# Kernel tuning notes

Measured on AMD Instinct MI355X. Metric: run time of the kernel, lower is better.

## Reference

```python
import jax, jax.numpy as jnp
import numpy as np

TEMPERATURE = 0.1
EPS = 1e-8

# MatchingRuleAllViews defaults:
#   intra_view_same_class=1, intra_view_different_class=0,
#   inter_view_same_class=1, inter_view_different_class=0,
#   inter_image_same_class=-1, inter_image_different_class=-1,
#   self_similarity=-1

def setup_inputs() -> dict:
    key = jax.random.key(0)
    k1, k2, k3 = jax.random.split(key, 3)
    B, V, C, HW = 2, 2, 64, 1024
    student = jax.random.normal(k1, (B, V, C, HW), dtype=jnp.float32)
    teacher = jax.random.normal(k2, (B, V, C, HW), dtype=jnp.float32)
    labels = jax.random.randint(k3, (B, V, HW), 0, 5, dtype=jnp.int32)
    return {"student_embeddings": student, "teacher_embeddings": teacher, "labels": labels}


def _masks(B, V, HW, labels_flat):
    # image / view / pixel ids for each of the N = B*V*HW flattened positions
    image_ids = jnp.repeat(jnp.arange(B), V * HW)          # [N]
    view_ids = jnp.tile(jnp.repeat(jnp.arange(V), HW), B)  # [N]
    pixel_ids = jnp.tile(jnp.arange(HW), B * V)            # [N]
    si = image_ids[:, None] == image_ids[None, :]
    sv = view_ids[:, None] == view_ids[None, :]
    sp = pixel_ids[:, None] == pixel_ids[None, :]
    sc = labels_flat[:, None] == labels_flat[None, :]
    # default rule: same image -> (same class ? 1 : 0); different image -> -1;
    # self-similarity (same image, view, pixel) -> -1
    mask = jnp.where(si, jnp.where(sc, 1, 0), -1)
    mask = jnp.where(si & sv & sp, -1, mask)
    numerator_mask = (mask == 1).astype(jnp.float32)
    denom_mask = (mask >= 0).astype(jnp.float32)
    return numerator_mask, denom_mask


def reference(student_embeddings, teacher_embeddings, labels):
    B, V, C, HW = student_embeddings.shape
    N = B * V * HW
    # [B,V,C,HW] -> [N,C], L2-normalized
    sf = student_embeddings.transpose(0, 1, 3, 2).reshape(N, C)
    tf = teacher_embeddings.transpose(0, 1, 3, 2).reshape(N, C)
    sf = sf / jnp.linalg.norm(sf, axis=1, keepdims=True).clip(1e-12)
    tf = tf / jnp.linalg.norm(tf, axis=1, keepdims=True).clip(1e-12)
    logits = (sf @ tf.T) / TEMPERATURE  # [N,N]

    labels_flat = labels.reshape(-1)
    numerator_mask, denom_mask = _masks(B, V, HW, labels_flat)

    # masked log-softmax over dim 1 (denominator restricted to denom_mask)
    masked_logits = jnp.where(denom_mask > 0, logits, -jnp.inf)
    log_prob = jax.nn.log_softmax(masked_logits, axis=1)
    log_prob = jnp.where(jnp.isneginf(log_prob), 0.0, log_prob)

    numerator_sums = numerator_mask.sum(1)
    mean_log_prob_pos = (numerator_mask * log_prob).sum(1) / (numerator_sums + EPS)
    valid = numerator_sums > EPS  # [N] bool
    n_valid = valid.sum().astype(jnp.float32)
    loss = -jnp.sum(jnp.where(valid, mean_log_prob_pos, 0.0)) / n_valid

    # bg_anchors=False branch: (loss * non_bg[valid]).sum() / (non_bg[valid].sum() + eps)
    non_bg = (labels_flat != 0).astype(jnp.float32)
    non_bg_valid_sum = jnp.sum(non_bg * valid.astype(jnp.float32))
    loss = (loss * non_bg_valid_sum) / (non_bg_valid_sum + EPS)
    return loss
```

## Files before the change

kernel.cpp:

```cpp
#include <hip/hip_runtime.h>
#include <math.h>

#define C_DIM 64
#define HW_DIM 1024
#define N_TOT 4096
#define IMG 2048
#define NEG_INF (-1e30f)

__global__ __launch_bounds__(256) void norms_kernel(
    const float* __restrict__ s, const float* __restrict__ t,
    float* __restrict__ rs, float* __restrict__ rt,
    float* __restrict__ accums) {
    const int b = blockIdx.x;
    const int pos = threadIdx.x & 63;
    const int chunk = threadIdx.x >> 6;
    const int n = ((b & 63) << 6) + pos;
    const float* __restrict__ src = (b >= 64) ? t : s;
    const int base = ((n >> 10) << 16) + (n & 1023);
    float ss = 0.f;
#pragma unroll
    for (int k = 0; k < 16; ++k) {
        float a = src[base + ((chunk << 4) + k) * HW_DIM];
        ss = fmaf(a, a, ss);
    }
    __shared__ float red[4][64];
    red[chunk][pos] = ss;
    __syncthreads();
    if (threadIdx.x < 64) {
        float v = red[0][pos] + red[1][pos] + red[2][pos] + red[3][pos];
        float r = 1.f / fmaxf(sqrtf(v), 1e-12f);
        if (b >= 64) rt[n] = r; else rs[n] = r;
    }
    if (b == 0 && threadIdx.x < 8) accums[threadIdx.x] = 0.f;
}

__global__ __launch_bounds__(256, 2) void logits_stats_kernel(
    const float* __restrict__ s, const float* __restrict__ t,
    const int* __restrict__ labels, const float* __restrict__ rs,
    const float* __restrict__ rt, float4* __restrict__ stats) {

    const int rb = blockIdx.x >> 3;
    const int jc = blockIdx.x & 7;
    const int img = rb >> 4;
    const int i0 = rb * 128;
    const int jbase0 = img * IMG + jc * 256;

    const int tid = threadIdx.x;
    const int tx = tid & 15;
    const int ty = tid >> 4;

    __shared__ __align__(16) float lds_a[C_DIM][132];
    __shared__ __align__(16) float lds_b[C_DIM][144];
    __shared__ __align__(16) float lds_rsa[128];
    __shared__ __align__(16) float lds_rtb[256];
    __shared__ __align__(16) int lds_labj[256];

    if (tid < 128) lds_rsa[tid] = rs[i0 + tid];
    lds_rtb[tid] = rt[jbase0 + tid];
    lds_labj[tid] = labels[jbase0 + tid];
    __syncthreads();

    {
        const int bvi = ((i0 >> 10) << 16) + (i0 & 1023);
        const int pos4 = (tid & 31) << 2;
        const int c0 = tid >> 5;
        float4 rv = *(const float4*)&lds_rsa[pos4];
#pragma unroll
        for (int k = 0; k < 8; ++k) {
            int c = c0 + (k << 3);
            float4 v = *(const float4*)(s + bvi + c * HW_DIM + pos4);
            v.x *= rv.x; v.y *= rv.y; v.z *= rv.z; v.w *= rv.w;
            *(float4*)&lds_a[c][pos4] = v;
        }
    }

    int lab_i[8];
#pragma unroll
    for (int rr = 0; rr < 8; ++rr) lab_i[rr] = labels[i0 + ty * 8 + rr];

    float m_run[8], s_run[8], A_run[8], c_run[8];
#pragma unroll
    for (int rr = 0; rr < 8; ++rr) {
        m_run[rr] = NEG_INF; s_run[rr] = 0.f; A_run[rr] = 0.f; c_run[rr] = 0.f;
    }

    const int arow = ty << 3;
    const int bo = tx << 3;
    const int bos = bo + ((bo >> 5) << 2);

    for (int jh = 0; jh < 2; ++jh) {
        const int colh = jh * 128;
        const int jb_img = jbase0 + colh;
        __syncthreads();
        {
            const int bvj = ((jb_img >> 10) << 16) + (jb_img & 1023);
            const int pos4 = (tid & 31) << 2;
            const int c0 = tid >> 5;
            float4 rv = *(const float4*)&lds_rtb[colh + pos4];
            const int sp = pos4 + ((pos4 >> 5) << 2);
#pragma unroll
            for (int k = 0; k < 8; ++k) {
                int c = c0 + (k << 3);
                float4 v = *(const float4*)(t + bvj + c * HW_DIM + pos4);
                v.x *= rv.x; v.y *= rv.y; v.z *= rv.z; v.w *= rv.w;
                *(float4*)&lds_b[c][sp] = v;
            }
        }
        __syncthreads();

        int labj[8];
        {
            int4 l0 = *(const int4*)&lds_labj[colh + bo];
            int4 l1 = *(const int4*)&lds_labj[colh + bo + 4];
            labj[0] = l0.x; labj[1] = l0.y; labj[2] = l0.z; labj[3] = l0.w;
            labj[4] = l1.x; labj[5] = l1.y; labj[6] = l1.z; labj[7] = l1.w;
        }

        float acc[8][8];
#pragma unroll
        for (int a = 0; a < 8; ++a)
#pragma unroll
            for (int b2 = 0; b2 < 8; ++b2) acc[a][b2] = 0.f;

#pragma unroll 4
        for (int c = 0; c < C_DIM; ++c) {
            float4 a0 = *(const float4*)&lds_a[c][arow];
            float4 a1 = *(const float4*)&lds_a[c][arow + 4];
            float4 b0 = *(const float4*)&lds_b[c][bos];
            float4 b1 = *(const float4*)&lds_b[c][bos + 4];
            const float ar[8] = {a0.x, a0.y, a0.z, a0.w, a1.x, a1.y, a1.z, a1.w};
            const float br[8] = {b0.x, b0.y, b0.z, b0.w, b1.x, b1.y, b1.z, b1.w};
#pragma unroll
            for (int a = 0; a < 8; ++a)
#pragma unroll
                for (int b2 = 0; b2 < 8; ++b2)
                    acc[a][b2] = fmaf(ar[a], br[b2], acc[a][b2]);
        }

#pragma unroll
        for (int rr = 0; rr < 8; ++rr) {
            const int i_g = i0 + arow + rr;
            const int li = lab_i[rr];
            float vals[8];
            float lm = NEG_INF;
#pragma unroll
            for (int jj = 0; jj < 8; ++jj) {
                const int j_g = jb_img + bo + jj;
                float logit = acc[rr][jj] * 10.f;
                bool self = (j_g == i_g);
                float v = self ? NEG_INF : logit;
                vals[jj] = v;
                lm = fmaxf(lm, v);
                if (!self && labj[jj] == li) {
                    A_run[rr] += logit;
                    c_run[rr] += 1.f;
                }
            }
            float M = fmaxf(m_run[rr], lm);
            float sn = s_run[rr] * __expf(m_run[rr] - M);
#pragma unroll
            for (int jj = 0; jj < 8; ++jj) sn += __expf(vals[jj] - M);
            m_run[rr] = M;
            s_run[rr] = sn;
        }
    }

#pragma unroll
    for (int off = 1; off < 16; off <<= 1) {
#pragma unroll
        for (int rr = 0; rr < 8; ++rr) {
            float m2 = __shfl_xor(m_run[rr], off, 64);
            float s2 = __shfl_xor(s_run[rr], off, 64);
            float A2 = __shfl_xor(A_run[rr], off, 64);
            float c2 = __shfl_xor(c_run[rr], off, 64);
            float M = fmaxf(m_run[rr], m2);
            s_run[rr] = s_run[rr] * __expf(m_run[rr] - M) + s2 * __expf(m2 - M);
            m_run[rr] = M;
            A_run[rr] += A2;
            c_run[rr] += c2;
        }
    }

    if (tx == 0) {
#pragma unroll
        for (int rr = 0; rr < 8; ++rr) {
            const int i_g = i0 + arow + rr;
            stats[i_g * 8 + jc] = make_float4(m_run[rr], s_run[rr], A_run[rr], c_run[rr]);
        }
    }
}

__global__ __launch_bounds__(256) void finalize_kernel(
    const float4* __restrict__ stats, const int* __restrict__ labels,
    float* __restrict__ accums, float* __restrict__ out) {
    const int tid = threadIdx.x;
    const int r = blockIdx.x * 256 + tid;

    float m = NEG_INF, sexp = 0.f, A = 0.f, cnt = 0.f;
#pragma unroll
    for (int c = 0; c < 8; ++c) {
        float4 v = stats[r * 8 + c];
        float M = fmaxf(m, v.x);
        sexp = sexp * __expf(m - M) + v.y * __expf(v.x - M);
        m = M;
        A += v.z;
        cnt += v.w;
    }
    float mlpp = 0.f, val = 0.f, nbv = 0.f;
    if (cnt > 0.5f) {
        float lse = m + __logf(sexp);
        mlpp = (A - cnt * lse) / (cnt + 1e-8f);
        val = 1.f;
        nbv = (labels[r] != 0) ? 1.f : 0.f;
    }

    __shared__ float red0[256], red1[256], red2[256];
    red0[tid] = mlpp; red1[tid] = val; red2[tid] = nbv;
    __syncthreads();
    for (int off = 128; off > 0; off >>= 1) {
        if (tid < off) {
            red0[tid] += red0[tid + off];
            red1[tid] += red1[tid + off];
            red2[tid] += red2[tid + off];
        }
        __syncthreads();
    }

    if (tid == 0) {
        atomicAdd(&accums[0], red0[0]);
        atomicAdd(&accums[1], red1[0]);
        atomicAdd(&accums[2], red2[0]);
        __threadfence();
        unsigned int old = atomicAdd((unsigned int*)&accums[3], 1u);
        if (old == 15u) {
            float S = atomicAdd(&accums[0], 0.f);
            float V = atomicAdd(&accums[1], 0.f);
            float NB = atomicAdd(&accums[2], 0.f);
            float loss = -S / V;
            out[0] = loss * NB / (NB + 1e-8f);
        }
    }
}

extern "C" void kernel_launch(void* const* d_in, const int* in_sizes, int n_in,
                              void* d_out, int out_size, void* d_ws, size_t ws_size,
                              hipStream_t stream) {
    const float* s = (const float*)d_in[0];
    const float* t = (const float*)d_in[1];
    const int* labels = (const int*)d_in[2];
    float* out = (float*)d_out;
    float* ws = (float*)d_ws;

    float* rs = ws;
    float* rt = ws + 4096;
    float* accums = ws + 8192;
    float4* stats = (float4*)(ws + 8208);

    hipLaunchKernelGGL(norms_kernel, dim3(128), dim3(256), 0, stream,
                       s, t, rs, rt, accums);
    hipLaunchKernelGGL(logits_stats_kernel, dim3(256), dim3(256), 0, stream,
                       s, t, labels, rs, rt, stats);
    hipLaunchKernelGGL(finalize_kernel, dim3(16), dim3(256), 0, stream,
                       stats, labels, accums, out);
}
```

Before: 85.83 us.

## Fuse norms, logits stats and finalize into one kernel with last-block reduction

Merges the three kernels into a single kernel. Each block computes its own inverse norms from the tiles it has staged in LDS, applies them as a per-element scale on the dot products, and the last block to finish (tracked with an atomic ticket) performs the final reduction. The grid is doubled to 512 blocks, each covering 128 columns instead of 256, which removes the inner two-pass column loop and adds parallelism. The goal is to cut launch overhead and the separate norm pass. In exchange it adds a memset call, recomputes norms redundantly in every block, and runs the finalize serially in one block over twice as many stats entries.

```diff
diff --git a/kernel.cpp b/kernel.cpp
--- a/kernel.cpp
+++ b/kernel.cpp
@@ -2,167 +2,130 @@
 #include <math.h>
 
 #define C_DIM 64
-#define HW_DIM 1024
-#define N_TOT 4096
-#define IMG 2048
 #define NEG_INF (-1e30f)
-
-__global__ __launch_bounds__(256) void norms_kernel(
+#define AW 132
+#define BW 140
+
+__global__ __launch_bounds__(256, 2) void fused_scl_kernel(
     const float* __restrict__ s, const float* __restrict__ t,
-    float* __restrict__ rs, float* __restrict__ rt,
-    float* __restrict__ accums) {
-    const int b = blockIdx.x;
-    const int pos = threadIdx.x & 63;
-    const int chunk = threadIdx.x >> 6;
-    const int n = ((b & 63) << 6) + pos;
-    const float* __restrict__ src = (b >= 64) ? t : s;
-    const int base = ((n >> 10) << 16) + (n & 1023);
-    float ss = 0.f;
-#pragma unroll
-    for (int k = 0; k < 16; ++k) {
-        float a = src[base + ((chunk << 4) + k) * HW_DIM];
-        ss = fmaf(a, a, ss);
-    }
-    __shared__ float red[4][64];
-    red[chunk][pos] = ss;
-    __syncthreads();
-    if (threadIdx.x < 64) {
-        float v = red[0][pos] + red[1][pos] + red[2][pos] + red[3][pos];
-        float r = 1.f / fmaxf(sqrtf(v), 1e-12f);
-        if (b >= 64) rt[n] = r; else rs[n] = r;
-    }
-    if (b == 0 && threadIdx.x < 8) accums[threadIdx.x] = 0.f;
-}
-
-__global__ __launch_bounds__(256, 2) void logits_stats_kernel(
-    const float* __restrict__ s, const float* __restrict__ t,
-    const int* __restrict__ labels, const float* __restrict__ rs,
-    const float* __restrict__ rt, float4* __restrict__ stats) {
-
-    const int rb = blockIdx.x >> 3;
-    const int jc = blockIdx.x & 7;
+    const int* __restrict__ labels, float4* __restrict__ stats,
+    unsigned int* __restrict__ ticket, float* __restrict__ out) {
+
+    const int rb = blockIdx.x >> 4;
+    const int jc = blockIdx.x & 15;
     const int img = rb >> 4;
     const int i0 = rb * 128;
-    const int jbase0 = img * IMG + jc * 256;
+    const int jb = img * 2048 + jc * 128;
 
     const int tid = threadIdx.x;
     const int tx = tid & 15;
     const int ty = tid >> 4;
 
-    __shared__ __align__(16) float lds_a[C_DIM][132];
-    __shared__ __align__(16) float lds_b[C_DIM][144];
-    __shared__ __align__(16) float lds_rsa[128];
-    __shared__ __align__(16) float lds_rtb[256];
-    __shared__ __align__(16) int lds_labj[256];
-
-    if (tid < 128) lds_rsa[tid] = rs[i0 + tid];
-    lds_rtb[tid] = rt[jbase0 + tid];
-    lds_labj[tid] = labels[jbase0 + tid];
-    __syncthreads();
+    __shared__ __align__(16) float lds_a[C_DIM][AW];
+    __shared__ __align__(16) float lds_b[C_DIM][BW];
+    __shared__ float lds_rs[128], lds_rt[128];
+    __shared__ int lds_labi[128], lds_labj[128];
+    __shared__ float red[3][256];
+    __shared__ int lds_last;
+
+    if (tid < 128) lds_labi[tid] = labels[i0 + tid];
+    else           lds_labj[tid - 128] = labels[jb + tid - 128];
 
     {
-        const int bvi = ((i0 >> 10) << 16) + (i0 & 1023);
         const int pos4 = (tid & 31) << 2;
         const int c0 = tid >> 5;
-        float4 rv = *(const float4*)&lds_rsa[pos4];
+        const int bvi = ((i0 >> 10) << 16) + (i0 & 1023) + pos4;
+        const int bvj = ((jb >> 10) << 16) + (jb & 1023) + pos4;
+        const int sp = pos4 + ((pos4 >> 5) << 2);
 #pragma unroll
         for (int k = 0; k < 8; ++k) {
             int c = c0 + (k << 3);
-            float4 v = *(const float4*)(s + bvi + c * HW_DIM + pos4);
-            v.x *= rv.x; v.y *= rv.y; v.z *= rv.z; v.w *= rv.w;
-            *(float4*)&lds_a[c][pos4] = v;
-        }
-    }
-
-    int lab_i[8];
-#pragma unroll
-    for (int rr = 0; rr < 8; ++rr) lab_i[rr] = labels[i0 + ty * 8 + rr];
-
-    float m_run[8], s_run[8], A_run[8], c_run[8];
-#pragma unroll
-    for (int rr = 0; rr < 8; ++rr) {
-        m_run[rr] = NEG_INF; s_run[rr] = 0.f; A_run[rr] = 0.f; c_run[rr] = 0.f;
-    }
+            *(float4*)&lds_a[c][pos4] = *(const float4*)(s + bvi + c * 1024);
+            *(float4*)&lds_b[c][sp]   = *(const float4*)(t + bvj + c * 1024);
+        }
+    }
+    __syncthreads();
+
+    {
+        const int p = tid & 127;
+        float ssq = 0.f;
+        if (tid < 128) {
+#pragma unroll
+            for (int c = 0; c < C_DIM; ++c) {
+                float v = lds_a[c][p];
+                ssq = fmaf(v, v, ssq);
+            }
+            lds_rs[p] = 1.f / fmaxf(sqrtf(ssq), 1e-12f);
+        } else {
+            const int sp = p + ((p >> 5) << 2);
+#pragma unroll
+            for (int c = 0; c < C_DIM; ++c) {
+                float v = lds_b[c][sp];
+                ssq = fmaf(v, v, ssq);
+            }
+            lds_rt[p] = 1.f / fmaxf(sqrtf(ssq), 1e-12f);
+        }
+    }
+    __syncthreads();
 
     const int arow = ty << 3;
     const int bo = tx << 3;
     const int bos = bo + ((bo >> 5) << 2);
 
-    for (int jh = 0; jh < 2; ++jh) {
-        const int colh = jh * 128;
-        const int jb_img = jbase0 + colh;
-        __syncthreads();
-        {
-            const int bvj = ((jb_img >> 10) << 16) + (jb_img & 1023);
-            const int pos4 = (tid & 31) << 2;
-            const int c0 = tid >> 5;
-            float4 rv = *(const float4*)&lds_rtb[colh + pos4];
-            const int sp = pos4 + ((pos4 >> 5) << 2);
-#pragma unroll
-            for (int k = 0; k < 8; ++k) {
-                int c = c0 + (k << 3);
-                float4 v = *(const float4*)(t + bvj + c * HW_DIM + pos4);
-                v.x *= rv.x; v.y *= rv.y; v.z *= rv.z; v.w *= rv.w;
-                *(float4*)&lds_b[c][sp] = v;
-            }
-        }
-        __syncthreads();
-
-        int labj[8];
-        {
-            int4 l0 = *(const int4*)&lds_labj[colh + bo];
-            int4 l1 = *(const int4*)&lds_labj[colh + bo + 4];
-            labj[0] = l0.x; labj[1] = l0.y; labj[2] = l0.z; labj[3] = l0.w;
-            labj[4] = l1.x; labj[5] = l1.y; labj[6] = l1.z; labj[7] = l1.w;
-        }
-
-        float acc[8][8];
+    float acc[8][8];
+#pragma unroll
+    for (int a = 0; a < 8; ++a)
+#pragma unroll
+        for (int b = 0; b < 8; ++b) acc[a][b] = 0.f;
+
+#pragma unroll 4
+    for (int c = 0; c < C_DIM; ++c) {
+        float4 a0 = *(const float4*)&lds_a[c][arow];
+        float4 a1 = *(const float4*)&lds_a[c][arow + 4];
+        float4 b0 = *(const float4*)&lds_b[c][bos];
+        float4 b1 = *(const float4*)&lds_b[c][bos + 4];
+        const float ar[8] = {a0.x, a0.y, a0.z, a0.w, a1.x, a1.y, a1.z, a1.w};
+        const float br[8] = {b0.x, b0.y, b0.z, b0.w, b1.x, b1.y, b1.z, b1.w};
 #pragma unroll
         for (int a = 0; a < 8; ++a)
 #pragma unroll
-            for (int b2 = 0; b2 < 8; ++b2) acc[a][b2] = 0.f;
-
-#pragma unroll 4
-        for (int c = 0; c < C_DIM; ++c) {
-            float4 a0 = *(const float4*)&lds_a[c][arow];
-            float4 a1 = *(const float4*)&lds_a[c][arow + 4];
-            float4 b0 = *(const float4*)&lds_b[c][bos];
-            float4 b1 = *(const float4*)&lds_b[c][bos + 4];
-            const float ar[8] = {a0.x, a0.y, a0.z, a0.w, a1.x, a1.y, a1.z, a1.w};
-            const float br[8] = {b0.x, b0.y, b0.z, b0.w, b1.x, b1.y, b1.z, b1.w};
-#pragma unroll
-            for (int a = 0; a < 8; ++a)
-#pragma unroll
-                for (int b2 = 0; b2 < 8; ++b2)
-                    acc[a][b2] = fmaf(ar[a], br[b2], acc[a][b2]);
-        }
-
-#pragma unroll
-        for (int rr = 0; rr < 8; ++rr) {
-            const int i_g = i0 + arow + rr;
-            const int li = lab_i[rr];
-            float vals[8];
-            float lm = NEG_INF;
-#pragma unroll
-            for (int jj = 0; jj < 8; ++jj) {
-                const int j_g = jb_img + bo + jj;
-                float logit = acc[rr][jj] * 10.f;
-                bool self = (j_g == i_g);
-                float v = self ? NEG_INF : logit;
-                vals[jj] = v;
-                lm = fmaxf(lm, v);
-                if (!self && labj[jj] == li) {
-                    A_run[rr] += logit;
-                    c_run[rr] += 1.f;
-                }
-            }
-            float M = fmaxf(m_run[rr], lm);
-            float sn = s_run[rr] * __expf(m_run[rr] - M);
-#pragma unroll
-            for (int jj = 0; jj < 8; ++jj) sn += __expf(vals[jj] - M);
-            m_run[rr] = M;
-            s_run[rr] = sn;
-        }
+            for (int b = 0; b < 8; ++b)
+                acc[a][b] = fmaf(ar[a], br[b], acc[a][b]);
+    }
+
+    int labi[8]; float rsi[8];
+#pragma unroll
+    for (int rr = 0; rr < 8; ++rr) {
+        labi[rr] = lds_labi[arow + rr];
+        rsi[rr] = lds_rs[arow + rr] * 10.f;
+    }
+    int labj[8]; float rtj[8];
+#pragma unroll
+    for (int jj = 0; jj < 8; ++jj) {
+        labj[jj] = lds_labj[bo + jj];
+        rtj[jj] = lds_rt[bo + jj];
+    }
+
+    float m_run[8], s_run[8], A_run[8], c_run[8];
+#pragma unroll
+    for (int rr = 0; rr < 8; ++rr) {
+        const int i_g = i0 + arow + rr;
+        float vals[8];
+        float lm = NEG_INF;
+        float A = 0.f, cn = 0.f;
+#pragma unroll
+        for (int jj = 0; jj < 8; ++jj) {
+            float logit = acc[rr][jj] * rsi[rr] * rtj[jj];
+            bool self = ((jb + bo + jj) == i_g);
+            float v = self ? NEG_INF : logit;
+            vals[jj] = v;
+            lm = fmaxf(lm, v);
+            if (!self && labj[jj] == labi[rr]) { A += logit; cn += 1.f; }
+        }
+        float sn = 0.f;
+#pragma unroll
+        for (int jj = 0; jj < 8; ++jj) sn += __expf(vals[jj] - lm);
+        m_run[rr] = lm; s_run[rr] = sn; A_run[rr] = A; c_run[rr] = cn;
     }
 
 #pragma unroll
@@ -183,62 +146,56 @@
 
     if (tx == 0) {
 #pragma unroll
-        for (int rr = 0; rr < 8; ++rr) {
-            const int i_g = i0 + arow + rr;
-            stats[i_g * 8 + jc] = make_float4(m_run[rr], s_run[rr], A_run[rr], c_run[rr]);
-        }
-    }
-}
-
-__global__ __launch_bounds__(256) void finalize_kernel(
-    const float4* __restrict__ stats, const int* __restrict__ labels,
-    float* __restrict__ accums, float* __restrict__ out) {
-    const int tid = threadIdx.x;
-    const int r = blockIdx.x * 256 + tid;
-
-    float m = NEG_INF, sexp = 0.f, A = 0.f, cnt = 0.f;
-#pragma unroll
-    for (int c = 0; c < 8; ++c) {
-        float4 v = stats[r * 8 + c];
-        float M = fmaxf(m, v.x);
-        sexp = sexp * __expf(m - M) + v.y * __expf(v.x - M);
-        m = M;
-        A += v.z;
-        cnt += v.w;
-    }
-    float mlpp = 0.f, val = 0.f, nbv = 0.f;
-    if (cnt > 0.5f) {
-        float lse = m + __logf(sexp);
-        mlpp = (A - cnt * lse) / (cnt + 1e-8f);
-        val = 1.f;
-        nbv = (labels[r] != 0) ? 1.f : 0.f;
-    }
-
-    __shared__ float red0[256], red1[256], red2[256];
-    red0[tid] = mlpp; red1[tid] = val; red2[tid] = nbv;
+        for (int rr = 0; rr < 8; ++rr)
+            stats[(i0 + arow + rr) * 16 + jc] =
+                make_float4(m_run[rr], s_run[rr], A_run[rr], c_run[rr]);
+        __threadfence();
+    }
+    __syncthreads();
+
+    if (tid == 0) {
+        unsigned int old = atomicAdd(ticket, 1u);
+        lds_last = (old == 511u) ? 1 : 0;
+    }
+    __syncthreads();
+    if (!lds_last) return;
+
+    __threadfence();
+    float sum_mlpp = 0.f, sum_valid = 0.f, sum_nbv = 0.f;
+#pragma unroll 2
+    for (int k = 0; k < 16; ++k) {
+        const int r = tid + (k << 8);
+        float m = NEG_INF, se = 0.f, A = 0.f, cnt = 0.f;
+#pragma unroll
+        for (int c = 0; c < 16; ++c) {
+            float4 v = stats[r * 16 + c];
+            float M = fmaxf(m, v.x);
+            se = se * __expf(m - M) + v.y * __expf(v.x - M);
+            m = M;
+            A += v.z;
+            cnt += v.w;
+        }
+        if (cnt > 0.5f) {
+            float lse = m + __logf(se);
+            sum_mlpp += (A - cnt * lse) / (cnt + 1e-8f);
+            sum_valid += 1.f;
+            if (labels[r] != 0) sum_nbv += 1.f;
+        }
+    }
+    red[0][tid] = sum_mlpp; red[1][tid] = sum_valid; red[2][tid] = sum_nbv;
     __syncthreads();
     for (int off = 128; off > 0; off >>= 1) {
         if (tid < off) {
-            red0[tid] += red0[tid + off];
-            red1[tid] += red1[tid + off];
-            red2[tid] += red2[tid + off];
+            red[0][tid] += red[0][tid + off];
+            red[1][tid] += red[1][tid + off];
+            red[2][tid] += red[2][tid + off];
         }
         __syncthreads();
     }
-
     if (tid == 0) {
-        atomicAdd(&accums[0], red0[0]);
-        atomicAdd(&accums[1], red1[0]);
-        atomicAdd(&accums[2], red2[0]);
-        __threadfence();
-        unsigned int old = atomicAdd((unsigned int*)&accums[3], 1u);
-        if (old == 15u) {
-            float S = atomicAdd(&accums[0], 0.f);
-            float V = atomicAdd(&accums[1], 0.f);
-            float NB = atomicAdd(&accums[2], 0.f);
-            float loss = -S / V;
-            out[0] = loss * NB / (NB + 1e-8f);
-        }
+        float loss = -red[0][0] / red[1][0];
+        float nbv = red[2][0];
+        out[0] = loss * nbv / (nbv + 1e-8f);
     }
 }
 
@@ -249,17 +206,11 @@
     const float* t = (const float*)d_in[1];
     const int* labels = (const int*)d_in[2];
     float* out = (float*)d_out;
-    float* ws = (float*)d_ws;
-
-    float* rs = ws;
-    float* rt = ws + 4096;
-    float* accums = ws + 8192;
-    float4* stats = (float4*)(ws + 8208);
-
-    hipLaunchKernelGGL(norms_kernel, dim3(128), dim3(256), 0, stream,
-                       s, t, rs, rt, accums);
-    hipLaunchKernelGGL(logits_stats_kernel, dim3(256), dim3(256), 0, stream,
-                       s, t, labels, rs, rt, stats);
-    hipLaunchKernelGGL(finalize_kernel, dim3(16), dim3(256), 0, stream,
-                       stats, labels, accums, out);
+
+    unsigned int* ticket = (unsigned int*)d_ws;
+    float4* stats = (float4*)((char*)d_ws + 16);
+
+    hipMemsetAsync(ticket, 0, 16, stream);
+    hipLaunchKernelGGL(fused_scl_kernel, dim3(512), dim3(256), 0, stream,
+                       s, t, labels, stats, ticket, out);
 }
```

Measured after the change: 186.3 us. 2.17x slower.
